# Optimization experiments

Hardware: AMD Instinct MI355X
Metric: run time of the kernel (lower is better)

Reference implementation:

```python
import jax, jax.numpy as jnp
import numpy as np

R_MAX = 5.0
NUM_BESSEL = 8
P_CUT = 5.0
NUM_GRAPHS = 32
AVG_NEIGH = 16.0
N_NODES = 40000
N_EDGES = 640000
NUM_ELEM = 10
CHANNELS = 32
# map each of the 9 spherical-harmonic components (l=0..2) to its l index
L_OF_LM = jnp.array([0, 1, 1, 1, 2, 2, 2, 2, 2])


def _sph(u):
    # component-normalized real spherical harmonics up to l=2 on unit vectors
    x, y, z = u[:, 0], u[:, 1], u[:, 2]
    s3, s15, s5 = jnp.sqrt(3.0), jnp.sqrt(15.0), jnp.sqrt(5.0)
    return jnp.stack([
        jnp.ones_like(x),
        s3 * x, s3 * y, s3 * z,
        s15 * x * y, s15 * y * z,
        (s5 / 2.0) * (3.0 * z * z - 1.0),
        s15 * x * z, (s15 / 2.0) * (x * x - y * y),
    ], axis=-1)  # [E, 9]


def _radial(lengths):
    # Bessel radial basis with smooth polynomial cutoff (p = P_CUT)
    u = lengths / R_MAX
    n = jnp.arange(1, NUM_BESSEL + 1, dtype=lengths.dtype)
    bessel = jnp.sqrt(2.0 / R_MAX) * jnp.sin(n * jnp.pi * u[:, None]) / lengths[:, None]
    p = P_CUT
    fc = (1.0 - (p + 1.0) * (p + 2.0) / 2.0 * u ** p
          + p * (p + 2.0) * u ** (p + 1.0)
          - p * (p + 1.0) / 2.0 * u ** (p + 2.0))
    fc = jnp.where(u < 1.0, fc, 0.0)
    return bessel * fc[:, None]  # [E, NUM_BESSEL]


def _layer(h, sh, edge_feats, sender, receiver, W1, W2, n_nodes):
    # radial MLP -> per-(l, channel) tensor-product weights
    tp_w = jax.nn.silu(edge_feats @ W1) @ W2          # [E, 3*C]
    tp_w = tp_w.reshape(-1, 3, CHANNELS)[:, L_OF_LM]  # [E, 9, C]
    # equivariant message: sh outer sender scalar feats, radially weighted
    m = sh[:, :, None] * h[sender][:, None, :] * tp_w  # [E, 9, C]
    A = jax.ops.segment_sum(m, receiver, num_segments=n_nodes) / AVG_NEIGH
    return A.at[:, 0, :].add(h)  # residual on the scalar (l=0) part


def _energy(positions, node_attrs, shifts, atomic_energies, W_embed,
            W1a, W2a, Wr1, W1b, W2b, Wm1, Wm2, edge_index, batch):
    sender, receiver = edge_index[0], edge_index[1]
    vec = positions[receiver] - positions[sender] + shifts  # [E, 3]
    lengths = jnp.sqrt(jnp.maximum(jnp.sum(vec * vec, -1), 1e-12))
    sh = _sph(vec / lengths[:, None])
    ef = _radial(lengths)
    n_nodes = positions.shape[0]
    e0 = node_attrs @ atomic_energies       # per-atom reference energies
    h = node_attrs @ W_embed                # LinearNodeEmbeddingBlock
    A1 = _layer(h, sh, ef, sender, receiver, W1a, W2a, n_nodes)
    e1 = (A1[:, 0, :] @ Wr1)[:, 0]          # LinearReadoutBlock
    A2 = _layer(A1[:, 0, :], sh, ef, sender, receiver, W1b, W2b, n_nodes)
    e2 = (jax.nn.silu(A2[:, 0, :] @ Wm1) @ Wm2)[:, 0]  # NonLinearReadoutBlock
    node_energy = e0 + e1 + e2
    total = jax.ops.segment_sum(node_energy, batch, num_segments=NUM_GRAPHS)
    return total, node_energy


def setup_inputs() -> dict:
    key = jax.random.key(0)
    ks = jax.random.split(key, 16)
    node_z = jax.random.randint(ks[0], (N_NODES,), 0, NUM_ELEM)
    node_attrs = jax.nn.one_hot(node_z, NUM_ELEM, dtype=jnp.float32)
    return {
        "positions": jax.random.normal(ks[1], (N_NODES, 3), jnp.float32) * 2.0,
        "node_attrs": node_attrs,
        "shifts": jnp.zeros((N_EDGES, 3), jnp.float32),
        "atomic_energies": jax.random.normal(ks[2], (NUM_ELEM,), jnp.float32),
        "W_embed": jax.random.normal(ks[3], (NUM_ELEM, CHANNELS), jnp.float32) / np.sqrt(NUM_ELEM),
        "W1a": jax.random.normal(ks[4], (NUM_BESSEL, 64), jnp.float32) / np.sqrt(NUM_BESSEL),
        "W2a": jax.random.normal(ks[5], (64, 3 * CHANNELS), jnp.float32) / 8.0,
        "Wr1": jax.random.normal(ks[6], (CHANNELS, 1), jnp.float32) / np.sqrt(CHANNELS),
        "W1b": jax.random.normal(ks[7], (NUM_BESSEL, 64), jnp.float32) / np.sqrt(NUM_BESSEL),
        "W2b": jax.random.normal(ks[8], (64, 3 * CHANNELS), jnp.float32) / 8.0,
        "Wm1": jax.random.normal(ks[9], (CHANNELS, 16), jnp.float32) / np.sqrt(CHANNELS),
        "Wm2": jax.random.normal(ks[10], (16, 1), jnp.float32) / 4.0,
        "edge_index": jax.random.randint(ks[11], (2, N_EDGES), 0, N_NODES).astype(jnp.int32),
        "batch": jnp.sort(jax.random.randint(ks[12], (N_NODES,), 0, NUM_GRAPHS)).astype(jnp.int32),
    }


def reference(positions, node_attrs, shifts, atomic_energies, W_embed,
              W1a, W2a, Wr1, W1b, W2b, Wm1, Wm2, edge_index, batch):
    def esum(pos):
        total, node_e = _energy(pos, node_attrs, shifts, atomic_energies, W_embed,
                                W1a, W2a, Wr1, W1b, W2b, Wm1, Wm2, edge_index, batch)
        return jnp.sum(total), (total, node_e)

    (_, (total, node_e)), g = jax.value_and_grad(esum, has_aux=True)(positions)
    forces = -g  # forces = -dE/dpositions, as in get_outputs
    return total, node_e, forces
```

## Files before the change

### kernel.cpp

```cpp
#include <hip/hip_runtime.h>
#include <math.h>

constexpr float R_MAX   = 5.0f;
constexpr float INV_R   = 0.2f;
constexpr float PI_F    = 3.14159265358979323846f;
constexpr float C0      = 0.632455532033675866f;
constexpr float INV_AVG = 1.0f / 16.0f;
constexpr int   TBL     = 4096;
constexpr int   SCHUNK  = 512;

__device__ __forceinline__ float sigm(float x) { return 1.0f / (1.0f + __expf(-x)); }

__device__ __forceinline__ unsigned f2bf(float x) {
    unsigned u = __float_as_uint(x);
    u += 0x7fffu + ((u >> 16) & 1u);
    return u >> 16;
}
__device__ __forceinline__ void store_bf_row(unsigned short* dst, const float* v) {
    uint4* o = (uint4*)dst;
#pragma unroll
    for (int w = 0; w < 4; w++) {
        uint4 t;
        t.x = f2bf(v[8*w+0]) | (f2bf(v[8*w+1]) << 16);
        t.y = f2bf(v[8*w+2]) | (f2bf(v[8*w+3]) << 16);
        t.z = f2bf(v[8*w+4]) | (f2bf(v[8*w+5]) << 16);
        t.w = f2bf(v[8*w+6]) | (f2bf(v[8*w+7]) << 16);
        o[w] = t;
    }
}
__device__ __forceinline__ void load_bf_row(const unsigned short* src, float* v) {
    const uint4* p = (const uint4*)src;
#pragma unroll
    for (int w = 0; w < 4; w++) {
        uint4 t = p[w];
        v[8*w+0] = __uint_as_float(t.x << 16);
        v[8*w+1] = __uint_as_float(t.x & 0xffff0000u);
        v[8*w+2] = __uint_as_float(t.y << 16);
        v[8*w+3] = __uint_as_float(t.y & 0xffff0000u);
        v[8*w+4] = __uint_as_float(t.z << 16);
        v[8*w+5] = __uint_as_float(t.z & 0xffff0000u);
        v[8*w+6] = __uint_as_float(t.w << 16);
        v[8*w+7] = __uint_as_float(t.w & 0xffff0000u);
    }
}

__device__ __forceinline__ void radial_ef_d(float u, float invL, float* ef, float* dd) {
    float u2 = u * u, u4 = u2 * u2, u5 = u4 * u;
    float fc  = 1.f - 21.f * u5 + 35.f * u5 * u - 15.f * u5 * u2;
    float om  = 1.f - u;
    float fcp = -105.f * u4 * om * om;
    float sp, cp;
    sincosf(PI_F * u, &sp, &cp);
    float twoc = 2.f * cp;
    float a = C0 * invL;
    float s_nm1 = 0.f, s_n = sp, c_nm1 = 1.f, c_n = cp;
#pragma unroll
    for (int n = 1; n <= 8; n++) {
        ef[n - 1] = a * s_n * fc;
        dd[n - 1] = a * fc * ((float)n * PI_F * INV_R * c_n - s_n * invL)
                  + a * s_n * fcp * INV_R;
        if (n < 8) {
            float sn2 = twoc * s_n - s_nm1; s_nm1 = s_n; s_n = sn2;
            float cn2 = twoc * c_n - c_nm1; c_nm1 = c_n; c_n = cn2;
        }
    }
}

__global__ __launch_bounds__(256) void k_table(
    const float* __restrict__ W1a, const float* __restrict__ W2a,
    const float* __restrict__ W1b, const float* __restrict__ W2b,
    float* __restrict__ twa, float* __restrict__ dta,
    float* __restrict__ twb, float* __restrict__ dtb,
    float* __restrict__ total)
{
    if (blockIdx.x == 0 && threadIdx.x < 32) total[threadIdx.x] = 0.f;
    int gid = blockIdx.x * 256 + threadIdx.x;
    if (gid >= (TBL + 1) * 16) return;
    int cg = gid & 7;
    int l  = (gid >> 3) & 1;
    int t  = gid >> 4;
    float u = fmaxf((float)t / (float)TBL, 1e-4f);
    float L = u * R_MAX;
    float invL = 1.f / L;
    float ef[8], dd[8], efu[8];
    radial_ef_d(u, invL, ef, dd);
#pragma unroll
    for (int k = 0; k < 8; k++) efu[k] = dd[k] * R_MAX;

    const float* W1 = l ? W1b : W1a;
    const float* W2 = l ? W2b : W2a;
    float*     tw_o = l ? twb : twa;
    float*     dt_o = l ? dtb : dta;
    float tw[4] = {0.f, 0.f, 0.f, 0.f};
    float dt[4] = {0.f, 0.f, 0.f, 0.f};
    for (int j = 0; j < 64; j++) {
        float s1 = 0.f, du = 0.f;
#pragma unroll
        for (int k = 0; k < 8; k++) {
            float w = W1[k * 64 + j];
            s1 += ef[k] * w; du += efu[k] * w;
        }
        float sg  = sigm(s1);
        float act = s1 * sg;
        float dj  = sg * (1.f + s1 * (1.f - sg)) * du;
        const float* w2 = W2 + j * 96 + cg * 4;
#pragma unroll
        for (int q = 0; q < 4; q++) {
            tw[q] += act * w2[q];
            dt[q] += dj * w2[q];
        }
    }
#pragma unroll
    for (int q = 0; q < 4; q++) {
        tw_o[(size_t)t * 32 + cg * 4 + q] = tw[q];
        dt_o[(size_t)t * 32 + cg * 4 + q] = dt[q];
    }
}

__global__ __launch_bounds__(256) void k_embed(
    const float* __restrict__ attrs, const float* __restrict__ ae,
    const float* __restrict__ Wemb, float* __restrict__ h,
    unsigned short* __restrict__ hA1_bf, float* __restrict__ e0,
    float* __restrict__ A1, float* __restrict__ forces,
    int* __restrict__ hist_r, int* __restrict__ hist_s, int N)
{
    int i = blockIdx.x * blockDim.x + threadIdx.x;
    if (i >= N) return;
    float a[10];
#pragma unroll
    for (int k = 0; k < 10; k++) a[k] = attrs[i * 10 + k];
    float e = 0.f;
#pragma unroll
    for (int k = 0; k < 10; k++) e += a[k] * ae[k];
    e0[i] = e;
    float v[32];
#pragma unroll
    for (int c = 0; c < 32; c++) {
        float t = 0.f;
#pragma unroll
        for (int k = 0; k < 10; k++) t += a[k] * Wemb[k * 32 + c];
        v[c] = t;
        h[i * 32 + c] = t;
        A1[i * 32 + c] = 0.f;
    }
    store_bf_row(hA1_bf + (size_t)i * 64, v);
    forces[3 * i + 0] = 0.f; forces[3 * i + 1] = 0.f; forces[3 * i + 2] = 0.f;
    hist_r[i] = 0; hist_s[i] = 0;
}

__global__ __launch_bounds__(256) void k_build(
    const float* __restrict__ pos, const float* __restrict__ shifts,
    const int* __restrict__ ei, int E,
    int* __restrict__ hist_r, int* __restrict__ hist_s,
    float4* __restrict__ urec)
{
    int e = blockIdx.x * 256 + threadIdx.x;
    if (e >= E) return;
    int s = ei[e], r = ei[E + e];
    float vx = pos[3 * r + 0] - pos[3 * s + 0] + shifts[3 * e + 0];
    float vy = pos[3 * r + 1] - pos[3 * s + 1] + shifts[3 * e + 1];
    float vz = pos[3 * r + 2] - pos[3 * s + 2] + shifts[3 * e + 2];
    float ss2 = vx * vx + vy * vy + vz * vz;
    float L = sqrtf(fmaxf(ss2, 1e-12f));
    if (L * INV_R < 1.f) {
        atomicAdd(&hist_r[r], 1);
        atomicAdd(&hist_s[s], 1);
        urec[e] = make_float4(vx, vy, vz,
                  __uint_as_float(((unsigned)s << 16) | (unsigned)r));
    } else {
        urec[e] = make_float4(0.f, 0.f, 0.f, __uint_as_float(0xFFFFFFFFu));
    }
}

__global__ __launch_bounds__(256) void k_scan_a(
    const int* __restrict__ hist_r, const int* __restrict__ hist_s,
    int n, int nb, int* __restrict__ part)
{
    __shared__ int red[256];
    int b = blockIdx.x;
    const int* hist = (b < nb) ? hist_r : hist_s;
    int cb = (b < nb) ? b : b - nb;
    int base = cb * SCHUNK;
    int t = threadIdx.x;
    int i0 = base + 2 * t, i1 = i0 + 1;
    int sum = 0;
    if (i0 < n) sum += hist[i0];
    if (i1 < n) sum += hist[i1];
    red[t] = sum;
    __syncthreads();
    for (int off = 128; off > 0; off >>= 1) {
        if (t < off) red[t] += red[t + off];
        __syncthreads();
    }
    if (t == 0) part[b] = red[0];
}

__global__ __launch_bounds__(256) void k_scan_b(
    const int* __restrict__ part, int nb, int* __restrict__ bbase,
    int* __restrict__ cnt)
{
    __shared__ int buf[512];
    int t = threadIdx.x;
    for (int k = t; k < 2 * nb; k += 256) buf[k] = part[k];
    __syncthreads();
    if (t < 2) {
        int base = t * nb;
        int run = 0;
        for (int k = 0; k < nb; k++) {
            int v = buf[base + k];
            buf[base + k] = run;
            run += v;
        }
        if (t == 0) *cnt = run;
    }
    __syncthreads();
    for (int k = t; k < 2 * nb; k += 256) bbase[k] = buf[k];
}

__global__ __launch_bounds__(256) void k_scan_c(
    const int* __restrict__ hist_r, const int* __restrict__ hist_s,
    int n, int nb, const int* __restrict__ bbase,
    int* __restrict__ cur_r, int* __restrict__ cur_s)
{
    __shared__ int sc[256];
    int b = blockIdx.x;
    const int* hist = (b < nb) ? hist_r : hist_s;
    int*       cur  = (b < nb) ? cur_r : cur_s;
    int cb = (b < nb) ? b : b - nb;
    int base = cb * SCHUNK;
    int t = threadIdx.x;
    int i0 = base + 2 * t, i1 = i0 + 1;
    int e0 = (i0 < n) ? hist[i0] : 0;
    int e1 = (i1 < n) ? hist[i1] : 0;
    int ts = e0 + e1;
    sc[t] = ts;
    __syncthreads();
    for (int off = 1; off < 256; off <<= 1) {
        int v = (t >= off) ? sc[t - off] : 0;
        __syncthreads();
        sc[t] += v;
        __syncthreads();
    }
    int excl = sc[t] - ts + bbase[b];
    if (i0 < n) cur[i0] = excl;
    if (i1 < n) cur[i1] = excl + e0;
}

__global__ __launch_bounds__(256) void k_sort(
    const float4* __restrict__ urec, int E,
    int* __restrict__ cur_r, int* __restrict__ cur_s,
    float4* __restrict__ rrec, float4* __restrict__ srec,
    int* __restrict__ map_sr)
{
    int e = blockIdx.x * 256 + threadIdx.x;
    if (e >= E) return;
    float4 uv = urec[e];
    unsigned pk = __float_as_uint(uv.w);
    if (pk == 0xFFFFFFFFu) return;
    int r = (int)(pk & 0xffffu);
    int s = (int)(pk >> 16);
    int rp = atomicAdd(&cur_r[r], 1);
    int sp = atomicAdd(&cur_s[s], 1);
    rrec[rp] = uv;
    srec[sp] = make_float4(uv.x, uv.y, uv.z,
               __uint_as_float(((unsigned)r << 16) | (unsigned)s));
    map_sr[sp] = rp;
}

__global__ __launch_bounds__(256) void k_edge_mlp_t(
    const float4* __restrict__ rec, const int* __restrict__ cnt,
    const float* __restrict__ tw_tbl, const unsigned short* __restrict__ feat,
    int fstride, float* __restrict__ acc)
{
    __shared__ float m_lds[256][33];
    __shared__ int   dst_lds[256];

    int na = *cnt;
    int tid = threadIdx.x;
    int stride = gridDim.x * 256;

    for (int base = blockIdx.x * 256; base < na; base += stride) {
        int i = base + tid;
        int dst = -1;
        if (i < na) {
            float4 rv = rec[i];
            unsigned pk = __float_as_uint(rv.w);
            int gn = pk >> 16;
            dst = (int)(pk & 0xffffu);
            float ss2 = rv.x * rv.x + rv.y * rv.y + rv.z * rv.z;
            float L = sqrtf(fmaxf(ss2, 1e-12f));
            float x = fminf(L * (INV_R * (float)TBL), (float)TBL - 1e-3f);
            int   i0 = (int)x;
            float f  = x - (float)i0;

            float fbuf[32];
            load_bf_row(feat + (size_t)gn * fstride, fbuf);

            const float4* r0 = (const float4*)(tw_tbl + (size_t)i0 * 32);
            const float4* r1 = r0 + 8;
#pragma unroll
            for (int q = 0; q < 8; q++) {
                float4 a = r0[q], b = r1[q];
                m_lds[tid][4 * q + 0] = fbuf[4*q+0] * (a.x + f * (b.x - a.x));
                m_lds[tid][4 * q + 1] = fbuf[4*q+1] * (a.y + f * (b.y - a.y));
                m_lds[tid][4 * q + 2] = fbuf[4*q+2] * (a.z + f * (b.z - a.z));
                m_lds[tid][4 * q + 3] = fbuf[4*q+3] * (a.w + f * (b.w - a.w));
            }
        }
        dst_lds[tid] = dst;
        __syncthreads();

        int grp = tid >> 5;
        int c   = tid & 31;
        int b32 = grp * 32;
        int cur = -1; float run = 0.f;
        for (int k = 0; k < 32; k++) {
            int d = dst_lds[b32 + k];
            if (d != cur) {
                if (cur >= 0) unsafeAtomicAdd(&acc[(size_t)cur * 32 + c], run);
                cur = d;
                run = (d >= 0) ? m_lds[b32 + k][c] : 0.f;
            } else if (d >= 0) {
                run += m_lds[b32 + k][c];
            }
        }
        if (cur >= 0) unsafeAtomicAdd(&acc[(size_t)cur * 32 + c], run);
        __syncthreads();
    }
}

__global__ __launch_bounds__(256) void k_node1(
    const float* __restrict__ h, float* __restrict__ A1,
    unsigned short* __restrict__ hA1_bf,
    const float* __restrict__ Wr1, float* __restrict__ e1,
    float* __restrict__ A2g2, int N)
{
    int i = blockIdx.x * blockDim.x + threadIdx.x;
    if (i >= N) return;
    float dot = 0.f;
    float v[32];
#pragma unroll
    for (int c = 0; c < 32; c++) {
        float t = A1[i * 32 + c] * INV_AVG + h[i * 32 + c];
        v[c] = t;
        A1[i * 32 + c] = t;
        A2g2[i * 32 + c] = 0.f;
        dot += t * Wr1[c];
    }
    e1[i] = dot;
    store_bf_row(hA1_bf + (size_t)i * 64 + 32, v);
}

__global__ __launch_bounds__(256) void k_node2(
    float* __restrict__ A2g2, unsigned short* __restrict__ g2_bf,
    const float* __restrict__ A1,
    const float* __restrict__ Wm1, const float* __restrict__ Wm2,
    const float* __restrict__ e0, const float* __restrict__ e1,
    float* __restrict__ node_e, float* __restrict__ total,
    float* __restrict__ g1, const int* __restrict__ batch, int N)
{
    __shared__ float bins[32];
    if (threadIdx.x < 32) bins[threadIdx.x] = 0.f;
    __syncthreads();
    int i = blockIdx.x * blockDim.x + threadIdx.x;
    if (i < N) {
        float A2[32];
#pragma unroll
        for (int c = 0; c < 32; c++) {
            A2[c] = A2g2[i * 32 + c] * INV_AVG + A1[i * 32 + c];
            g1[i * 32 + c] = 0.f;
        }
        float z[16];
#pragma unroll
        for (int k = 0; k < 16; k++) {
            float v = 0.f;
#pragma unroll
            for (int c = 0; c < 32; c++) v += A2[c] * Wm1[c * 16 + k];
            z[k] = v;
        }
        float e2 = 0.f;
        float wk[16];
#pragma unroll
        for (int k = 0; k < 16; k++) {
            float sg = sigm(z[k]);
            float m2 = Wm2[k];
            e2 += z[k] * sg * m2;
            wk[k] = m2 * sg * (1.f + z[k] * (1.f - sg));
        }
        float g2v[32];
#pragma unroll
        for (int c = 0; c < 32; c++) {
            float v = 0.f;
#pragma unroll
            for (int k = 0; k < 16; k++) v += Wm1[c * 16 + k] * wk[k];
            g2v[c] = v;
            A2g2[i * 32 + c] = v;
        }
        store_bf_row(g2_bf + (size_t)i * 32, g2v);
        float ne = e0[i] + e1[i] + e2;
        node_e[i] = ne;
        atomicAdd(&bins[batch[i]], ne);
    }
    __syncthreads();
    if (threadIdx.x < 32) unsafeAtomicAdd(&total[threadIdx.x], bins[threadIdx.x]);
}

__global__ __launch_bounds__(256) void k_node3(
    float* __restrict__ g1, const float* __restrict__ g2,
    const float* __restrict__ Wr1, int N)
{
    int i = blockIdx.x * blockDim.x + threadIdx.x;
    if (i >= N) return;
#pragma unroll
    for (int c = 0; c < 32; c++)
        g1[i * 32 + c] = g1[i * 32 + c] * INV_AVG + g2[i * 32 + c] + Wr1[c];
}

__global__ __launch_bounds__(256) void k_force_r(
    const float4* __restrict__ rec, const int* __restrict__ cnt,
    const float* __restrict__ dta, const float* __restrict__ dtb,
    const unsigned short* __restrict__ hA1_bf,
    const float* __restrict__ g1, const float* __restrict__ g2,
    float* __restrict__ forces, float* __restrict__ sc_buf)
{
    __shared__ float f_lds[256][4];
    __shared__ int   dst_lds[256];

    int na = *cnt;
    int tid = threadIdx.x;
    int stride = gridDim.x * 256;

    for (int base = blockIdx.x * 256; base < na; base += stride) {
        int i = base + tid;
        int dstf = -1;
        float fx = 0.f, fy = 0.f, fz = 0.f;

        if (i < na) {
            float4 rv = rec[i];
            unsigned pk = __float_as_uint(rv.w);
            int r = (int)(pk & 0xffffu);
            int s = (int)(pk >> 16);
            float vx = rv.x, vy = rv.y, vz = rv.z;
            float ss2 = vx * vx + vy * vy + vz * vz;
            float scv = 0.f;
            if (ss2 > 1e-12f) {
                float L = sqrtf(ss2);
                float invL = 1.f / L;
                float x = fminf(L * (INV_R * (float)TBL), (float)TBL - 1e-3f);
                int   i0 = (int)x;
                float f  = x - (float)i0;

                float hb[32], ab[32];
                const unsigned short* row = hA1_bf + (size_t)s * 64;
                load_bf_row(row, hb);
                load_bf_row(row + 32, ab);

                const float4* a0 = (const float4*)(dta + (size_t)i0 * 32);
                const float4* a1 = a0 + 8;
                const float4* b0 = (const float4*)(dtb + (size_t)i0 * 32);
                const float4* b1 = b0 + 8;
                const float4* pa = (const float4*)(g1 + (size_t)r * 32);
                const float4* pc = (const float4*)(g2 + (size_t)r * 32);

                float dot = 0.f;
#pragma unroll
                for (int q = 0; q < 8; q++) {
                    float4 xg = pa[q], t0 = a0[q], t1 = a1[q];
                    dot += xg.x * hb[4*q+0] * (t0.x + f * (t1.x - t0.x))
                         + xg.y * hb[4*q+1] * (t0.y + f * (t1.y - t0.y))
                         + xg.z * hb[4*q+2] * (t0.z + f * (t1.z - t0.z))
                         + xg.w * hb[4*q+3] * (t0.w + f * (t1.w - t0.w));
                }
#pragma unroll
                for (int q = 0; q < 8; q++) {
                    float4 xg = pc[q], t0 = b0[q], t1 = b1[q];
                    dot += xg.x * ab[4*q+0] * (t0.x + f * (t1.x - t0.x))
                         + xg.y * ab[4*q+1] * (t0.y + f * (t1.y - t0.y))
                         + xg.z * ab[4*q+2] * (t0.z + f * (t1.z - t0.z))
                         + xg.w * ab[4*q+3] * (t0.w + f * (t1.w - t0.w));
                }

                scv = INV_AVG * INV_R * dot * invL;
                fx = -scv * vx; fy = -scv * vy; fz = -scv * vz;
                dstf = r;
            }
            sc_buf[i] = scv;
        }
        f_lds[tid][0] = fx; f_lds[tid][1] = fy; f_lds[tid][2] = fz;
        dst_lds[tid] = dstf;
        __syncthreads();

        int grp = tid >> 5;
        int c   = tid & 31;
        if (c < 3) {
            int b32 = grp * 32;
            int cur = -1; float run = 0.f;
            for (int k = 0; k < 32; k++) {
                int d = dst_lds[b32 + k];
                if (d != cur) {
                    if (cur >= 0) unsafeAtomicAdd(&forces[3 * cur + c], run);
                    cur = d;
                    run = (d >= 0) ? f_lds[b32 + k][c] : 0.f;
                } else if (d >= 0) {
                    run += f_lds[b32 + k][c];
                }
            }
            if (cur >= 0) unsafeAtomicAdd(&forces[3 * cur + c], run);
        }
        __syncthreads();
    }
}

__global__ __launch_bounds__(256) void k_force_s2(
    const float4* __restrict__ rec, const int* __restrict__ cnt,
    const int* __restrict__ map_sr, const float* __restrict__ sc_buf,
    float* __restrict__ forces)
{
    __shared__ float f_lds[256][4];
    __shared__ int   dst_lds[256];

    int na = *cnt;
    int tid = threadIdx.x;
    int stride = gridDim.x * 256;

    for (int base = blockIdx.x * 256; base < na; base += stride) {
        int i = base + tid;
        int dstf = -1;
        float fx = 0.f, fy = 0.f, fz = 0.f;
        if (i < na) {
            float4 rv = rec[i];
            unsigned pk = __float_as_uint(rv.w);
            float scv = sc_buf[map_sr[i]];
            fx = scv * rv.x; fy = scv * rv.y; fz = scv * rv.z;
            dstf = (int)(pk & 0xffffu);
        }
        f_lds[tid][0] = fx; f_lds[tid][1] = fy; f_lds[tid][2] = fz;
        dst_lds[tid] = dstf;
        __syncthreads();

        int grp = tid >> 5;
        int c   = tid & 31;
        if (c < 3) {
            int b32 = grp * 32;
            int cur = -1; float run = 0.f;
            for (int k = 0; k < 32; k++) {
                int d = dst_lds[b32 + k];
                if (d != cur) {
                    if (cur >= 0) unsafeAtomicAdd(&forces[3 * cur + c], run);
                    cur = d;
                    run = (d >= 0) ? f_lds[b32 + k][c] : 0.f;
                } else if (d >= 0) {
                    run += f_lds[b32 + k][c];
                }
            }
            if (cur >= 0) unsafeAtomicAdd(&forces[3 * cur + c], run);
        }
        __syncthreads();
    }
}

extern "C" void kernel_launch(void* const* d_in, const int* in_sizes, int n_in,
                              void* d_out, int out_size, void* d_ws, size_t ws_size,
                              hipStream_t stream)
{
    const float* pos    = (const float*)d_in[0];
    const float* attrs  = (const float*)d_in[1];
    const float* shifts = (const float*)d_in[2];
    const float* ae     = (const float*)d_in[3];
    const float* Wemb   = (const float*)d_in[4];
    const float* W1a    = (const float*)d_in[5];
    const float* W2a    = (const float*)d_in[6];
    const float* Wr1    = (const float*)d_in[7];
    const float* W1b    = (const float*)d_in[8];
    const float* W2b    = (const float*)d_in[9];
    const float* Wm1    = (const float*)d_in[10];
    const float* Wm2    = (const float*)d_in[11];
    const int*   ei     = (const int*)d_in[12];
    const int*   batch  = (const int*)d_in[13];

    int N = in_sizes[13];
    int E = in_sizes[12] / 2;

    float* out    = (float*)d_out;
    float* total  = out;
    float* node_e = out + 32;
    float* forces = out + 32 + N;

    float* ws = (float*)d_ws;
    size_t NC = (size_t)N * 32;
    float* h    = ws;
    float* A1   = h  + NC;
    float* A2g2 = A1 + NC;
    float* g1   = A2g2 + NC;
    float* e0   = g1 + NC;
    float* e1   = e0 + N;
    int* hist_r = (int*)(e1 + N);
    int* hist_s = hist_r + N;
    int* cur_r  = hist_s + N;
    int* cur_s  = cur_r + N;
    int* cnt    = cur_s + N;
    size_t ioff = ((size_t)(cnt + 1 - (int*)ws) + 3) & ~(size_t)3;
    float4* rrec = (float4*)(ws + ioff);
    float4* srec = rrec + E;
    float* tbl  = (float*)(srec + E);
    size_t tstride = (size_t)(TBL + 1) * 32;
    float* twa = tbl;
    float* dta = twa + tstride;
    float* twb = dta + tstride;
    float* dtb = twb + tstride;
    int*   map_sr = (int*)(dtb + tstride);
    float* sc_buf = (float*)(map_sr + E);
    unsigned short* hA1_bf = (unsigned short*)(sc_buf + E);
    unsigned short* g2_bf  = hA1_bf + 2 * NC;
    int* part  = (int*)(g2_bf + NC);
    int* bbase = part + 1024;
    float4* urec = (float4*)A2g2;

    int nb_n = (N + 255) / 256;
    int nb_e = (E + 255) / 256;
    int nb_g = nb_e < 2048 ? nb_e : 2048;
    int nb_t = ((TBL + 1) * 16 + 255) / 256;
    int nbs  = (N + SCHUNK - 1) / SCHUNK;

    k_table<<<nb_t, 256, 0, stream>>>(W1a, W2a, W1b, W2b, twa, dta, twb, dtb,
                                      total);
    k_embed<<<nb_n, 256, 0, stream>>>(attrs, ae, Wemb, h, hA1_bf, e0,
                                      A1, forces, hist_r, hist_s, N);
    k_build<<<nb_e, 256, 0, stream>>>(pos, shifts, ei, E, hist_r, hist_s, urec);
    k_scan_a<<<2 * nbs, 256, 0, stream>>>(hist_r, hist_s, N, nbs, part);
    k_scan_b<<<1, 256, 0, stream>>>(part, nbs, bbase, cnt);
    k_scan_c<<<2 * nbs, 256, 0, stream>>>(hist_r, hist_s, N, nbs, bbase,
                                          cur_r, cur_s);
    k_sort<<<nb_e, 256, 0, stream>>>(urec, E, cur_r, cur_s, rrec, srec, map_sr);

    k_edge_mlp_t<<<nb_g, 256, 0, stream>>>(rrec, cnt, twa, hA1_bf, 64, A1);
    k_node1<<<nb_n, 256, 0, stream>>>(h, A1, hA1_bf, Wr1, e1, A2g2, N);
    k_edge_mlp_t<<<nb_g, 256, 0, stream>>>(rrec, cnt, twb, hA1_bf + 32, 64, A2g2);
    k_node2<<<nb_n, 256, 0, stream>>>(A2g2, g2_bf, A1, Wm1, Wm2, e0, e1,
                                      node_e, total, g1, batch, N);
    k_edge_mlp_t<<<nb_g, 256, 0, stream>>>(srec, cnt, twb, g2_bf, 32, g1);
    k_node3<<<nb_n, 256, 0, stream>>>(g1, A2g2, Wr1, N);
    k_force_r<<<nb_g, 256, 0, stream>>>(rrec, cnt, dta, dtb, hA1_bf,
                                        g1, A2g2, forces, sc_buf);
    k_force_s2<<<nb_g, 256, 0, stream>>>(srec, cnt, map_sr, sc_buf, forces);
}
```

Before: 328.2 us.

## Merge setup kernels and fuse layer-b force term into sender-sorted MLP pass

```diff
diff --git a/kernel.cpp b/kernel.cpp
--- a/kernel.cpp
+++ b/kernel.cpp
@@ -66,109 +66,105 @@
     }
 }
 
-__global__ __launch_bounds__(256) void k_table(
+__global__ __launch_bounds__(256) void k_setup(
     const float* __restrict__ W1a, const float* __restrict__ W2a,
     const float* __restrict__ W1b, const float* __restrict__ W2b,
     float* __restrict__ twa, float* __restrict__ dta,
     float* __restrict__ twb, float* __restrict__ dtb,
-    float* __restrict__ total)
-{
-    if (blockIdx.x == 0 && threadIdx.x < 32) total[threadIdx.x] = 0.f;
-    int gid = blockIdx.x * 256 + threadIdx.x;
-    if (gid >= (TBL + 1) * 16) return;
-    int cg = gid & 7;
-    int l  = (gid >> 3) & 1;
-    int t  = gid >> 4;
-    float u = fmaxf((float)t / (float)TBL, 1e-4f);
-    float L = u * R_MAX;
-    float invL = 1.f / L;
-    float ef[8], dd[8], efu[8];
-    radial_ef_d(u, invL, ef, dd);
-#pragma unroll
-    for (int k = 0; k < 8; k++) efu[k] = dd[k] * R_MAX;
-
-    const float* W1 = l ? W1b : W1a;
-    const float* W2 = l ? W2b : W2a;
-    float*     tw_o = l ? twb : twa;
-    float*     dt_o = l ? dtb : dta;
-    float tw[4] = {0.f, 0.f, 0.f, 0.f};
-    float dt[4] = {0.f, 0.f, 0.f, 0.f};
-    for (int j = 0; j < 64; j++) {
-        float s1 = 0.f, du = 0.f;
-#pragma unroll
-        for (int k = 0; k < 8; k++) {
-            float w = W1[k * 64 + j];
-            s1 += ef[k] * w; du += efu[k] * w;
-        }
-        float sg  = sigm(s1);
-        float act = s1 * sg;
-        float dj  = sg * (1.f + s1 * (1.f - sg)) * du;
-        const float* w2 = W2 + j * 96 + cg * 4;
-#pragma unroll
-        for (int q = 0; q < 4; q++) {
-            tw[q] += act * w2[q];
-            dt[q] += dj * w2[q];
-        }
-    }
-#pragma unroll
-    for (int q = 0; q < 4; q++) {
-        tw_o[(size_t)t * 32 + cg * 4 + q] = tw[q];
-        dt_o[(size_t)t * 32 + cg * 4 + q] = dt[q];
-    }
-}
-
-__global__ __launch_bounds__(256) void k_embed(
+    float* __restrict__ total,
     const float* __restrict__ attrs, const float* __restrict__ ae,
     const float* __restrict__ Wemb, float* __restrict__ h,
     unsigned short* __restrict__ hA1_bf, float* __restrict__ e0,
-    float* __restrict__ A1, float* __restrict__ forces,
-    int* __restrict__ hist_r, int* __restrict__ hist_s, int N)
-{
-    int i = blockIdx.x * blockDim.x + threadIdx.x;
-    if (i >= N) return;
-    float a[10];
-#pragma unroll
-    for (int k = 0; k < 10; k++) a[k] = attrs[i * 10 + k];
-    float e = 0.f;
-#pragma unroll
-    for (int k = 0; k < 10; k++) e += a[k] * ae[k];
-    e0[i] = e;
-    float v[32];
-#pragma unroll
-    for (int c = 0; c < 32; c++) {
-        float t = 0.f;
-#pragma unroll
-        for (int k = 0; k < 10; k++) t += a[k] * Wemb[k * 32 + c];
-        v[c] = t;
-        h[i * 32 + c] = t;
-        A1[i * 32 + c] = 0.f;
-    }
-    store_bf_row(hA1_bf + (size_t)i * 64, v);
-    forces[3 * i + 0] = 0.f; forces[3 * i + 1] = 0.f; forces[3 * i + 2] = 0.f;
-    hist_r[i] = 0; hist_s[i] = 0;
-}
-
-__global__ __launch_bounds__(256) void k_build(
+    float* __restrict__ A1, float* __restrict__ forces, int N,
     const float* __restrict__ pos, const float* __restrict__ shifts,
     const int* __restrict__ ei, int E,
     int* __restrict__ hist_r, int* __restrict__ hist_s,
-    float4* __restrict__ urec)
-{
-    int e = blockIdx.x * 256 + threadIdx.x;
-    if (e >= E) return;
-    int s = ei[e], r = ei[E + e];
-    float vx = pos[3 * r + 0] - pos[3 * s + 0] + shifts[3 * e + 0];
-    float vy = pos[3 * r + 1] - pos[3 * s + 1] + shifts[3 * e + 1];
-    float vz = pos[3 * r + 2] - pos[3 * s + 2] + shifts[3 * e + 2];
-    float ss2 = vx * vx + vy * vy + vz * vz;
-    float L = sqrtf(fmaxf(ss2, 1e-12f));
-    if (L * INV_R < 1.f) {
-        atomicAdd(&hist_r[r], 1);
-        atomicAdd(&hist_s[s], 1);
-        urec[e] = make_float4(vx, vy, vz,
-                  __uint_as_float(((unsigned)s << 16) | (unsigned)r));
+    float4* __restrict__ urec,
+    int nbt, int nbn)
+{
+    int b = blockIdx.x;
+    if (b < nbt) {
+        if (b == 0 && threadIdx.x < 32) total[threadIdx.x] = 0.f;
+        int gid = b * 256 + threadIdx.x;
+        if (gid >= (TBL + 1) * 16) return;
+        int cg = gid & 7;
+        int l  = (gid >> 3) & 1;
+        int t  = gid >> 4;
+        float u = fmaxf((float)t / (float)TBL, 1e-4f);
+        float L = u * R_MAX;
+        float invL = 1.f / L;
+        float ef[8], dd[8], efu[8];
+        radial_ef_d(u, invL, ef, dd);
+#pragma unroll
+        for (int k = 0; k < 8; k++) efu[k] = dd[k] * R_MAX;
+        const float* W1 = l ? W1b : W1a;
+        const float* W2 = l ? W2b : W2a;
+        float*     tw_o = l ? twb : twa;
+        float*     dt_o = l ? dtb : dta;
+        float tw[4] = {0.f, 0.f, 0.f, 0.f};
+        float dt[4] = {0.f, 0.f, 0.f, 0.f};
+        for (int j = 0; j < 64; j++) {
+            float s1 = 0.f, du = 0.f;
+#pragma unroll
+            for (int k = 0; k < 8; k++) {
+                float w = W1[k * 64 + j];
+                s1 += ef[k] * w; du += efu[k] * w;
+            }
+            float sg  = sigm(s1);
+            float act = s1 * sg;
+            float dj  = sg * (1.f + s1 * (1.f - sg)) * du;
+            const float* w2 = W2 + j * 96 + cg * 4;
+#pragma unroll
+            for (int q = 0; q < 4; q++) {
+                tw[q] += act * w2[q];
+                dt[q] += dj * w2[q];
+            }
+        }
+#pragma unroll
+        for (int q = 0; q < 4; q++) {
+            tw_o[(size_t)t * 32 + cg * 4 + q] = tw[q];
+            dt_o[(size_t)t * 32 + cg * 4 + q] = dt[q];
+        }
+    } else if (b < nbt + nbn) {
+        int i = (b - nbt) * 256 + threadIdx.x;
+        if (i >= N) return;
+        float a[10];
+#pragma unroll
+        for (int k = 0; k < 10; k++) a[k] = attrs[i * 10 + k];
+        float e = 0.f;
+#pragma unroll
+        for (int k = 0; k < 10; k++) e += a[k] * ae[k];
+        e0[i] = e;
+        float v[32];
+#pragma unroll
+        for (int c = 0; c < 32; c++) {
+            float t = 0.f;
+#pragma unroll
+            for (int k = 0; k < 10; k++) t += a[k] * Wemb[k * 32 + c];
+            v[c] = t;
+            h[i * 32 + c] = t;
+            A1[i * 32 + c] = 0.f;
+        }
+        store_bf_row(hA1_bf + (size_t)i * 64, v);
+        forces[3*i+0] = 0.f; forces[3*i+1] = 0.f; forces[3*i+2] = 0.f;
+        hist_r[i] = 0; hist_s[i] = 0;
     } else {
-        urec[e] = make_float4(0.f, 0.f, 0.f, __uint_as_float(0xFFFFFFFFu));
+        int e = (b - nbt - nbn) * 256 + threadIdx.x;
+        if (e >= E) return;
+        int s = ei[e], r = ei[E + e];
+        float vx = pos[3*r+0] - pos[3*s+0] + shifts[3*e+0];
+        float vy = pos[3*r+1] - pos[3*s+1] + shifts[3*e+1];
+        float vz = pos[3*r+2] - pos[3*s+2] + shifts[3*e+2];
+        float ss2 = vx*vx + vy*vy + vz*vz;
+        float L = sqrtf(fmaxf(ss2, 1e-12f));
+        if (L * INV_R < 1.f) {
+            atomicAdd(&hist_r[r], 1);
+            atomicAdd(&hist_s[s], 1);
+            urec[e] = make_float4(vx, vy, vz,
+                      __uint_as_float(((unsigned)s << 16) | (unsigned)r));
+        } else {
+            urec[e] = make_float4(0.f, 0.f, 0.f, __uint_as_float(0xFFFFFFFFu));
+        }
     }
 }
 
@@ -405,30 +401,99 @@
     if (threadIdx.x < 32) unsafeAtomicAdd(&total[threadIdx.x], bins[threadIdx.x]);
 }
 
-__global__ __launch_bounds__(256) void k_node3(
-    float* __restrict__ g1, const float* __restrict__ g2,
-    const float* __restrict__ Wr1, int N)
-{
-    int i = blockIdx.x * blockDim.x + threadIdx.x;
-    if (i >= N) return;
-#pragma unroll
-    for (int c = 0; c < 32; c++)
-        g1[i * 32 + c] = g1[i * 32 + c] * INV_AVG + g2[i * 32 + c] + Wr1[c];
-}
-
-__global__ __launch_bounds__(256) void k_force_r(
+__global__ __launch_bounds__(256) void k_mlp3fb(
     const float4* __restrict__ rec, const int* __restrict__ cnt,
-    const float* __restrict__ dta, const float* __restrict__ dtb,
+    const float* __restrict__ tw_tbl, const float* __restrict__ dt_tbl,
+    const unsigned short* __restrict__ g2_bf,
     const unsigned short* __restrict__ hA1_bf,
-    const float* __restrict__ g1, const float* __restrict__ g2,
-    float* __restrict__ forces, float* __restrict__ sc_buf)
-{
-    __shared__ float f_lds[256][4];
+    const int* __restrict__ map_sr,
+    float* __restrict__ g1acc, float* __restrict__ dotb_buf)
+{
+    __shared__ float m_lds[256][33];
     __shared__ int   dst_lds[256];
 
     int na = *cnt;
     int tid = threadIdx.x;
     int stride = gridDim.x * 256;
+
+    for (int base = blockIdx.x * 256; base < na; base += stride) {
+        int i = base + tid;
+        int dst = -1;
+        if (i < na) {
+            float4 rv = rec[i];
+            unsigned pk = __float_as_uint(rv.w);
+            int r = (int)(pk >> 16);
+            dst = (int)(pk & 0xffffu);
+            float ss2 = rv.x * rv.x + rv.y * rv.y + rv.z * rv.z;
+            float L = sqrtf(fmaxf(ss2, 1e-12f));
+            float x = fminf(L * (INV_R * (float)TBL), (float)TBL - 1e-3f);
+            int   i0 = (int)x;
+            float f  = x - (float)i0;
+
+            float gb[32], ab[32];
+            load_bf_row(g2_bf + (size_t)r * 32, gb);
+            load_bf_row(hA1_bf + (size_t)dst * 64 + 32, ab);
+
+            const float4* r0 = (const float4*)(tw_tbl + (size_t)i0 * 32);
+            const float4* r1 = r0 + 8;
+            const float4* d0 = (const float4*)(dt_tbl + (size_t)i0 * 32);
+            const float4* d1 = d0 + 8;
+            float dotb = 0.f;
+#pragma unroll
+            for (int q = 0; q < 8; q++) {
+                float4 a = r0[q], b = r1[q], da = d0[q], db = d1[q];
+                float t0 = a.x + f * (b.x - a.x);
+                float t1 = a.y + f * (b.y - a.y);
+                float t2 = a.z + f * (b.z - a.z);
+                float t3 = a.w + f * (b.w - a.w);
+                m_lds[tid][4*q+0] = gb[4*q+0] * t0;
+                m_lds[tid][4*q+1] = gb[4*q+1] * t1;
+                m_lds[tid][4*q+2] = gb[4*q+2] * t2;
+                m_lds[tid][4*q+3] = gb[4*q+3] * t3;
+                dotb += gb[4*q+0] * ab[4*q+0] * (da.x + f * (db.x - da.x))
+                      + gb[4*q+1] * ab[4*q+1] * (da.y + f * (db.y - da.y))
+                      + gb[4*q+2] * ab[4*q+2] * (da.z + f * (db.z - da.z))
+                      + gb[4*q+3] * ab[4*q+3] * (da.w + f * (db.w - da.w));
+            }
+            dotb_buf[map_sr[i]] = dotb;
+        }
+        dst_lds[tid] = dst;
+        __syncthreads();
+
+        int grp = tid >> 5;
+        int c   = tid & 31;
+        int b32 = grp * 32;
+        int cur = -1; float run = 0.f;
+        for (int k = 0; k < 32; k++) {
+            int d = dst_lds[b32 + k];
+            if (d != cur) {
+                if (cur >= 0) unsafeAtomicAdd(&g1acc[(size_t)cur * 32 + c], run);
+                cur = d;
+                run = (d >= 0) ? m_lds[b32 + k][c] : 0.f;
+            } else if (d >= 0) {
+                run += m_lds[b32 + k][c];
+            }
+        }
+        if (cur >= 0) unsafeAtomicAdd(&g1acc[(size_t)cur * 32 + c], run);
+        __syncthreads();
+    }
+}
+
+__global__ __launch_bounds__(256) void k_force_ra(
+    const float4* __restrict__ rec, const int* __restrict__ cnt,
+    const float* __restrict__ dta,
+    const unsigned short* __restrict__ hA1_bf,
+    const float* __restrict__ g1acc, const float* __restrict__ g2,
+    const float* __restrict__ Wr1, const float* __restrict__ dotb_buf,
+    float* __restrict__ forces, float* __restrict__ sc_buf)
+{
+    __shared__ float f_lds[256][4];
+    __shared__ int   dst_lds[256];
+
+    int na = *cnt;
+    int tid = threadIdx.x;
+    int stride = gridDim.x * 256;
+    const float4* w4 = (const float4*)Wr1;
 
     for (int base = blockIdx.x * 256; base < na; base += stride) {
         int i = base + tid;
@@ -450,34 +515,27 @@
                 int   i0 = (int)x;
                 float f  = x - (float)i0;
 
-                float hb[32], ab[32];
-                const unsigned short* row = hA1_bf + (size_t)s * 64;
-                load_bf_row(row, hb);
-                load_bf_row(row + 32, ab);
+                float hb[32];
+                load_bf_row(hA1_bf + (size_t)s * 64, hb);
 
                 const float4* a0 = (const float4*)(dta + (size_t)i0 * 32);
                 const float4* a1 = a0 + 8;
-                const float4* b0 = (const float4*)(dtb + (size_t)i0 * 32);
-                const float4* b1 = b0 + 8;
-                const float4* pa = (const float4*)(g1 + (size_t)r * 32);
+                const float4* pa = (const float4*)(g1acc + (size_t)r * 32);
                 const float4* pc = (const float4*)(g2 + (size_t)r * 32);
 
-                float dot = 0.f;
+                float dot = dotb_buf[i];
 #pragma unroll
                 for (int q = 0; q < 8; q++) {
-                    float4 xg = pa[q], t0 = a0[q], t1 = a1[q];
-                    dot += xg.x * hb[4*q+0] * (t0.x + f * (t1.x - t0.x))
-                         + xg.y * hb[4*q+1] * (t0.y + f * (t1.y - t0.y))
-                         + xg.z * hb[4*q+2] * (t0.z + f * (t1.z - t0.z))
-                         + xg.w * hb[4*q+3] * (t0.w + f * (t1.w - t0.w));
-                }
-#pragma unroll
-                for (int q = 0; q < 8; q++) {
-                    float4 xg = pc[q], t0 = b0[q], t1 = b1[q];
-                    dot += xg.x * ab[4*q+0] * (t0.x + f * (t1.x - t0.x))
-                         + xg.y * ab[4*q+1] * (t0.y + f * (t1.y - t0.y))
-                         + xg.z * ab[4*q+2] * (t0.z + f * (t1.z - t0.z))
-                         + xg.w * ab[4*q+3] * (t0.w + f * (t1.w - t0.w));
+                    float4 ga = pa[q], gc = pc[q], wr = w4[q];
+                    float4 t0 = a0[q], t1 = a1[q];
+                    float g0 = ga.x * INV_AVG + gc.x + wr.x;
+                    float g1v = ga.y * INV_AVG + gc.y + wr.y;
+                    float g2v = ga.z * INV_AVG + gc.z + wr.z;
+                    float g3 = ga.w * INV_AVG + gc.w + wr.w;
+                    dot += g0 * hb[4*q+0] * (t0.x + f * (t1.x - t0.x))
+                         + g1v * hb[4*q+1] * (t0.y + f * (t1.y - t0.y))
+                         + g2v * hb[4*q+2] * (t0.z + f * (t1.z - t0.z))
+                         + g3 * hb[4*q+3] * (t0.w + f * (t1.w - t0.w));
                 }
 
                 scv = INV_AVG * INV_R * dot * invL;
@@ -614,6 +672,7 @@
     unsigned short* g2_bf  = hA1_bf + 2 * NC;
     int* part  = (int*)(g2_bf + NC);
     int* bbase = part + 1024;
+    float* dotb_buf = (float*)(bbase + 1024);
     float4* urec = (float4*)A2g2;
 
     int nb_n = (N + 255) / 256;
@@ -622,11 +681,10 @@
     int nb_t = ((TBL + 1) * 16 + 255) / 256;
     int nbs  = (N + SCHUNK - 1) / SCHUNK;
 
-    k_table<<<nb_t, 256, 0, stream>>>(W1a, W2a, W1b, W2b, twa, dta, twb, dtb,
-                                      total);
-    k_embed<<<nb_n, 256, 0, stream>>>(attrs, ae, Wemb, h, hA1_bf, e0,
-                                      A1, forces, hist_r, hist_s, N);
-    k_build<<<nb_e, 256, 0, stream>>>(pos, shifts, ei, E, hist_r, hist_s, urec);
+    k_setup<<<nb_t + nb_n + nb_e, 256, 0, stream>>>(
+        W1a, W2a, W1b, W2b, twa, dta, twb, dtb, total,
+        attrs, ae, Wemb, h, hA1_bf, e0, A1, forces, N,
+        pos, shifts, ei, E, hist_r, hist_s, urec, nb_t, nb_n);
     k_scan_a<<<2 * nbs, 256, 0, stream>>>(hist_r, hist_s, N, nbs, part);
     k_scan_b<<<1, 256, 0, stream>>>(part, nbs, bbase, cnt);
     k_scan_c<<<2 * nbs, 256, 0, stream>>>(hist_r, hist_s, N, nbs, bbase,
@@ -638,9 +696,10 @@
     k_edge_mlp_t<<<nb_g, 256, 0, stream>>>(rrec, cnt, twb, hA1_bf + 32, 64, A2g2);
     k_node2<<<nb_n, 256, 0, stream>>>(A2g2, g2_bf, A1, Wm1, Wm2, e0, e1,
                                       node_e, total, g1, batch, N);
-    k_edge_mlp_t<<<nb_g, 256, 0, stream>>>(srec, cnt, twb, g2_bf, 32, g1);
-    k_node3<<<nb_n, 256, 0, stream>>>(g1, A2g2, Wr1, N);
-    k_force_r<<<nb_g, 256, 0, stream>>>(rrec, cnt, dta, dtb, hA1_bf,
-                                        g1, A2g2, forces, sc_buf);
+    k_mlp3fb<<<nb_g, 256, 0, stream>>>(srec, cnt, twb, dtb, g2_bf, hA1_bf,
+                                       map_sr, g1, dotb_buf);
+    k_force_ra<<<nb_g, 256, 0, stream>>>(rrec, cnt, dta, hA1_bf,
+                                         g1, A2g2, Wr1, dotb_buf,
+                                         forces, sc_buf);
     k_force_s2<<<nb_g, 256, 0, stream>>>(srec, cnt, map_sr, sc_buf, forces);
 }
```

Measured after the change: 271.0 us. -17.4%, faster.
